# Optimization experiments

Hardware: AMD Instinct MI355X
Metric: run time of the kernel (lower is better)

## Reference

```python
import jax, jax.numpy as jnp
import numpy as np

NEG_INF = -1.0e9  # matches torch masked_fill value

def setup_inputs() -> dict:
    key = jax.random.key(0)
    kq, kk, kv, km = jax.random.split(key, 4)
    B, S, D = 16, 2048, 128
    query = jax.random.normal(kq, (B, S, D), dtype=jnp.float32)
    k = jax.random.normal(kk, (B, S, D), dtype=jnp.float32)
    value = jax.random.normal(kv, (B, S, D), dtype=jnp.float32)
    mask = jax.random.randint(km, (B, S, S), 0, 2).astype(jnp.bool_)
    return {"query": query, "key": k, "value": value, "mask": mask}

def reference(query, key, value, mask):
    # scores: [B, Sq, Sk]
    D = key.shape[-1]
    scale = jnp.sqrt(jnp.asarray(D, dtype=query.dtype))
    scores = jnp.einsum('bqd,bkd->bqk', query, key) / scale
    scores = jnp.where(mask, jnp.asarray(NEG_INF, dtype=scores.dtype), scores)
    attn = jax.nn.softmax(scores, axis=2)
    # dropout p=0.0 -> identity in eval/reference
    out = jnp.einsum('bqk,bkd->bqd', attn, value)
    return out, attn
```

## Files before the change

### kernel.cpp

```cpp
#include <hip/hip_runtime.h>

#define S 2048
#define Dh 128
#define NB 16
#define OUT_ELEMS ((size_t)NB * S * Dh)
#define NEG_BIG -1.0e9f
#define SCALE 0.08838834764831845f

typedef __attribute__((ext_vector_type(8))) short bf16x8;
typedef __attribute__((ext_vector_type(4))) float f32x4;
typedef __attribute__((ext_vector_type(4))) short s16x4;

__device__ __forceinline__ short f2bf(float x) {
    unsigned u = __float_as_uint(x);
    u += 0x7fffu + ((u >> 16) & 1u);
    return (short)(u >> 16);
}

__device__ __forceinline__ s16x4 pack4(float4 v) {
    s16x4 r;
    r.x = f2bf(v.x); r.y = f2bf(v.y); r.z = f2bf(v.z); r.w = f2bf(v.w);
    return r;
}

__global__ void detect_mask(const unsigned char* __restrict__ m, int* __restrict__ flag) {
    __shared__ int any;
    if (threadIdx.x == 0) any = 0;
    __syncthreads();
    int t = threadIdx.x;
    unsigned char v = (unsigned char)(m[t * 4 + 1] | m[t * 4 + 2] | m[t * 4 + 3]);
    if (v) atomicOr(&any, 1);
    __syncthreads();
    if (t == 0) *flag = any;
}

__global__ __launch_bounds__(256) void transpose_v(const float* __restrict__ V,
                                                   short* __restrict__ Vt) {
    const int kb = blockIdx.x, b = blockIdx.y;
    const float* Vb = V + ((size_t)b * S + kb * 64) * Dh;
    short* VtB = Vt + (size_t)b * Dh * S;
    __shared__ float Ls[64][132];
    const int t = threadIdx.x;
#pragma unroll
    for (int i = 0; i < 8; i++) {
        int idx = t + i * 256;
        int r = idx >> 5, c = (idx & 31) << 2;
        *(float4*)&Ls[r][c] = *(const float4*)(Vb + r * Dh + c);
    }
    __syncthreads();
#pragma unroll
    for (int i = 0; i < 8; i++) {
        int idx = t + i * 256;
        int n = idx >> 4, kc = (idx & 15) << 2;
        s16x4 o;
        o.x = f2bf(Ls[kc + 0][n]);
        o.y = f2bf(Ls[kc + 1][n]);
        o.z = f2bf(Ls[kc + 2][n]);
        o.w = f2bf(Ls[kc + 3][n]);
        *(s16x4*)(VtB + (size_t)n * S + kb * 64 + kc) = o;
    }
}

__global__ __launch_bounds__(256) void cvt_bf16(const float* __restrict__ in,
                                                short* __restrict__ out) {
    const size_t n4 = (size_t)NB * S * Dh / 4;
    for (size_t i = (size_t)blockIdx.x * 256 + threadIdx.x; i < n4; i += (size_t)gridDim.x * 256) {
        float4 v = ((const float4*)in)[i];
        ((s16x4*)out)[i] = pack4(v);
    }
}

__global__ __launch_bounds__(256, 2) void flash_pv(const short* __restrict__ Qbf,
                                                   const short* __restrict__ Kbf,
                                                   const short* __restrict__ Vt,
                                                   const void* __restrict__ maskp,
                                                   const int* __restrict__ flagp,
                                                   float2* __restrict__ stats,
                                                   float* __restrict__ Out) {
    const int bid = blockIdx.x;
    const int xcd = bid & 7, kk = bid >> 3;
    const int b = xcd * 2 + (kk >> 5), qt = kk & 31;

    const short* QbfB = Qbf + ((size_t)b * S + qt * 64) * Dh;
    const short* KbfB = Kbf + (size_t)b * S * Dh;
    const short* VtB  = Vt  + (size_t)b * Dh * S;
    float* OutB = Out + ((size_t)b * S + qt * 64) * Dh;
    const int flag = *flagp;

    __shared__ short Qs[2][64][72];
    __shared__ short Ks[2][128][72];
    __shared__ short Ps[2][64][72];
    __shared__ __align__(16) unsigned char Msk[64][128];

    const int t = threadIdx.x, w = t >> 6, lane = t & 63, fr = lane & 15, quad = lane >> 4;
    const int mo = w * 16;

#pragma unroll
    for (int i = 0; i < 4; i++) {
        int idx = t + i * 256;
        int r = idx >> 4, c8 = (idx & 15) * 8;
        *(bf16x8*)&Qs[c8 >> 6][r][c8 & 63] = *(const bf16x8*)(QbfB + (size_t)r * Dh + c8);
    }

    float m[4], l[4];
#pragma unroll
    for (int r = 0; r < 4; r++) { m[r] = -3.4e38f; l[r] = 0.f; }
    f32x4 acc_o[8] = {};

    bf16x8 kv[8];
    int4 mreg[2];
#pragma unroll
    for (int i = 0; i < 8; i++) {
        int idx = t + i * 256;
        int r = idx >> 4, c8 = (idx & 15) * 8;
        kv[i] = *(const bf16x8*)(KbfB + (size_t)r * Dh + c8);
    }
    if (flag) {
        const unsigned char* Mb = (const unsigned char*)maskp + ((size_t)b * S + qt * 64) * S;
#pragma unroll
        for (int i = 0; i < 2; i++) {
            int idx = t + i * 256;
            int r = idx >> 3, c16 = (idx & 7) * 16;
            mreg[i] = *(const int4*)(Mb + (size_t)r * S + c16);
        }
    }

    for (int kt = 0; kt < 16; kt++) {
        __syncthreads();
#pragma unroll
        for (int i = 0; i < 8; i++) {
            int idx = t + i * 256;
            int r = idx >> 4, c8 = (idx & 15) * 8;
            *(bf16x8*)&Ks[c8 >> 6][r][c8 & 63] = kv[i];
        }
        if (flag) {
#pragma unroll
            for (int i = 0; i < 2; i++) {
                int idx = t + i * 256;
                int r = idx >> 3, c16 = (idx & 7) * 16;
                *(int4*)&Msk[r][c16] = mreg[i];
            }
        } else {
            const int* Mb = (const int*)maskp + ((size_t)b * S + qt * 64) * S + (size_t)kt * 128;
#pragma unroll
            for (int i = 0; i < 8; i++) {
                int idx = t + i * 256;
                int r = idx >> 5, c4 = (idx & 31) * 4;
                int4 mv = *(const int4*)(Mb + (size_t)r * S + c4);
                uchar4 o;
                o.x = (unsigned char)(mv.x != 0);
                o.y = (unsigned char)(mv.y != 0);
                o.z = (unsigned char)(mv.z != 0);
                o.w = (unsigned char)(mv.w != 0);
                *(uchar4*)&Msk[r][c4] = o;
            }
        }
        __syncthreads();

        if (kt < 15) {
#pragma unroll
            for (int i = 0; i < 8; i++) {
                int idx = t + i * 256;
                int r = idx >> 4, c8 = (idx & 15) * 8;
                kv[i] = *(const bf16x8*)(KbfB + (size_t)((kt + 1) * 128 + r) * Dh + c8);
            }
            if (flag) {
                const unsigned char* Mb = (const unsigned char*)maskp + ((size_t)b * S + qt * 64) * S + (size_t)(kt + 1) * 128;
#pragma unroll
                for (int i = 0; i < 2; i++) {
                    int idx = t + i * 256;
                    int r = idx >> 3, c16 = (idx & 7) * 16;
                    mreg[i] = *(const int4*)(Mb + (size_t)r * S + c16);
                }
            }
        }

        f32x4 acc_s[8] = {};
#pragma unroll
        for (int ks = 0; ks < 4; ks++) {
            const int h = ks >> 1, o = (ks & 1) * 32 + quad * 8;
            bf16x8 af = *(const bf16x8*)&Qs[h][mo + fr][o];
            bf16x8 bfv[8];
#pragma unroll
            for (int ni = 0; ni < 8; ni++) bfv[ni] = *(const bf16x8*)&Ks[h][ni * 16 + fr][o];
#pragma unroll
            for (int ni = 0; ni < 8; ni++)
                acc_s[ni] = __builtin_amdgcn_mfma_f32_16x16x32_bf16(af, bfv[ni], acc_s[ni], 0, 0, 0);
        }

#pragma unroll
        for (int r = 0; r < 4; r++) {
            const int row = mo + quad * 4 + r;
            float s[8];
#pragma unroll
            for (int ni = 0; ni < 8; ni++) {
                float v = acc_s[ni][r] * SCALE;
                if (Msk[row][ni * 16 + fr]) v = NEG_BIG;
                s[ni] = v;
            }
            float mx = s[0];
#pragma unroll
            for (int ni = 1; ni < 8; ni++) mx = fmaxf(mx, s[ni]);
#pragma unroll
            for (int o = 8; o > 0; o >>= 1) mx = fmaxf(mx, __shfl_xor(mx, o, 64));
            const float mn = fmaxf(m[r], mx);
            const float f = __expf(m[r] - mn);
            float p[8], lt = 0.f;
#pragma unroll
            for (int ni = 0; ni < 8; ni++) { p[ni] = __expf(s[ni] - mn); lt += p[ni]; }
#pragma unroll
            for (int o = 8; o > 0; o >>= 1) lt += __shfl_xor(lt, o, 64);
            l[r] = l[r] * f + lt;
            m[r] = mn;
#pragma unroll
            for (int ni = 0; ni < 8; ni++) acc_o[ni][r] *= f;
#pragma unroll
            for (int ni = 0; ni < 8; ni++) {
                const int col = ni * 16 + fr;
                Ps[col >> 6][row][col & 63] = f2bf(p[ni]);
            }
        }
        __syncthreads();

#pragma unroll
        for (int ks = 0; ks < 4; ks++) {
            const int h = ks >> 1, o = (ks & 1) * 32 + quad * 8;
            bf16x8 paf = *(const bf16x8*)&Ps[h][mo + fr][o];
            bf16x8 pb[8];
#pragma unroll
            for (int ni = 0; ni < 8; ni++)
                pb[ni] = *(const bf16x8*)(VtB + (size_t)(ni * 16 + fr) * S + kt * 128 + ks * 32 + quad * 8);
#pragma unroll
            for (int ni = 0; ni < 8; ni++)
                acc_o[ni] = __builtin_amdgcn_mfma_f32_16x16x32_bf16(paf, pb[ni], acc_o[ni], 0, 0, 0);
        }
    }

    float invl[4];
#pragma unroll
    for (int r = 0; r < 4; r++) invl[r] = 1.0f / l[r];
#pragma unroll
    for (int ni = 0; ni < 8; ni++)
#pragma unroll
        for (int r = 0; r < 4; r++) {
            const int row = mo + quad * 4 + r;
            OutB[(size_t)row * Dh + ni * 16 + fr] = acc_o[ni][r] * invl[r];
        }
    if (fr == 0) {
#pragma unroll
        for (int r = 0; r < 4; r++)
            stats[(size_t)b * S + qt * 64 + mo + quad * 4 + r] = make_float2(m[r], invl[r]);
    }
}

__global__ __launch_bounds__(256, 2) void attn_write(const short* __restrict__ Qbf,
                                                     const short* __restrict__ Kbf,
                                                     const void* __restrict__ maskp,
                                                     const int* __restrict__ flagp,
                                                     const float2* __restrict__ stats,
                                                     float* __restrict__ Attn) {
    const int bid = blockIdx.x;
    const int xcd = bid & 7, kk = bid >> 3;
    const int b = xcd * 2 + (kk >> 8), rem = kk & 255, qt = rem >> 4, kt = rem & 15;

    const short* Qb = Qbf + ((size_t)b * S + qt * 128) * Dh;
    const short* Kb = Kbf + ((size_t)b * S + kt * 128) * Dh;
    __shared__ short As[128][72];
    __shared__ short Bs[128][72];
    __shared__ __align__(16) unsigned char Ms[128][144];
    const int t = threadIdx.x;
    const int w = t >> 6, lane = t & 63, fr = lane & 15, quad = lane >> 4;
    const int mw = (w >> 1) * 64, nw = (w & 1) * 64;
    f32x4 acc[4][4] = {};

    const int flag = *flagp;
    if (flag) {
        const unsigned char* Mb = (const unsigned char*)maskp + ((size_t)b * S + qt * 128) * S + (size_t)kt * 128;
#pragma unroll
        for (int i = 0; i < 4; i++) {
            int idx = t + i * 256;
            int r = idx >> 3, c = (idx & 7) * 16;
            *(int4*)&Ms[r][c] = *(const int4*)(Mb + (size_t)r * S + c);
        }
    } else {
        const int* Mb = (const int*)maskp + ((size_t)b * S + qt * 128) * S + (size_t)kt * 128;
#pragma unroll
        for (int i = 0; i < 16; i++) {
            int idx = t + i * 256;
            int r = idx >> 5, c = (idx & 31) * 4;
            int4 mv = *(const int4*)(Mb + (size_t)r * S + c);
            uchar4 o;
            o.x = (unsigned char)(mv.x != 0);
            o.y = (unsigned char)(mv.y != 0);
            o.z = (unsigned char)(mv.z != 0);
            o.w = (unsigned char)(mv.w != 0);
            *(uchar4*)&Ms[r][c] = o;
        }
    }

    float2 st[4][4];
#pragma unroll
    for (int mi = 0; mi < 4; mi++)
#pragma unroll
        for (int r = 0; r < 4; r++)
            st[mi][r] = stats[(size_t)b * S + qt * 128 + mw + mi * 16 + quad * 4 + r];

    for (int k0 = 0; k0 < Dh; k0 += 64) {
        __syncthreads();
#pragma unroll
        for (int i = 0; i < 4; i++) {
            int idx = t + i * 256;
            int r = idx >> 3, c8 = (idx & 7) * 8;
            *(bf16x8*)&As[r][c8] = *(const bf16x8*)(Qb + (size_t)r * Dh + k0 + c8);
            *(bf16x8*)&Bs[r][c8] = *(const bf16x8*)(Kb + (size_t)r * Dh + k0 + c8);
        }
        __syncthreads();
#pragma unroll
        for (int kc = 0; kc < 2; kc++) {
            const int ko = kc * 32 + quad * 8;
            bf16x8 af[4], bf[4];
#pragma unroll
            for (int mi = 0; mi < 4; mi++) af[mi] = *(const bf16x8*)&As[mw + mi * 16 + fr][ko];
#pragma unroll
            for (int ni = 0; ni < 4; ni++) bf[ni] = *(const bf16x8*)&Bs[nw + ni * 16 + fr][ko];
#pragma unroll
            for (int mi = 0; mi < 4; mi++)
#pragma unroll
                for (int ni = 0; ni < 4; ni++)
                    acc[mi][ni] = __builtin_amdgcn_mfma_f32_16x16x32_bf16(af[mi], bf[ni], acc[mi][ni], 0, 0, 0);
        }
    }

    float* AttnB = Attn + (size_t)b * S * S;
#pragma unroll
    for (int mi = 0; mi < 4; mi++)
#pragma unroll
        for (int ni = 0; ni < 4; ni++)
#pragma unroll
            for (int r = 0; r < 4; r++) {
                const int lrow = mw + mi * 16 + quad * 4 + r;
                const int lcol = nw + ni * 16 + fr;
                float v = acc[mi][ni][r] * SCALE;
                if (Ms[lrow][lcol]) v = NEG_BIG;
                const float p = __expf(v - st[mi][r].x) * st[mi][r].y;
                AttnB[(size_t)(qt * 128 + lrow) * S + kt * 128 + lcol] = p;
            }
}

__global__ __launch_bounds__(256) void reduce_stats(const float2* __restrict__ part,
                                                    float2* __restrict__ stats) {
    const int rid = blockIdx.x * 256 + threadIdx.x;
    const int b = rid >> 11, row = rid & (S - 1);
    float2 p[16];
    float M = -3.4e38f;
#pragma unroll
    for (int kt = 0; kt < 16; kt++) {
        p[kt] = part[((size_t)(b * 16 + kt)) * S + row];
        M = fmaxf(M, p[kt].x);
    }
    float L = 0.f;
#pragma unroll
    for (int kt = 0; kt < 16; kt++) L += p[kt].y * __expf(p[kt].x - M);
    stats[rid] = make_float2(M, 1.0f / L);
}

__global__ __launch_bounds__(256, 2) void qk_kernel(const float* __restrict__ Q,
                                                    const float* __restrict__ Km,
                                                    float* __restrict__ Sc,
                                                    const void* __restrict__ maskp,
                                                    const int* __restrict__ flagp,
                                                    float2* __restrict__ part,
                                                    const int fuse) {
    const int kt = blockIdx.x, qt = blockIdx.y, b = blockIdx.z;
    const float* Qb = Q + ((size_t)b * S + qt * 128) * Dh;
    const float* Kb = Km + ((size_t)b * S + kt * 128) * Dh;
    __shared__ short As[128][72];
    __shared__ short Bs[128][72];
    __shared__ __align__(16) unsigned char Ms[128][144];
    const int t = threadIdx.x;
    const int w = t >> 6, lane = t & 63, fr = lane & 15, quad = lane >> 4;
    const int mw = (w >> 1) * 64, nw = (w & 1) * 64;
    f32x4 acc[4][4] = {};

    if (fuse) {
        const int flag = *flagp;
        if (flag) {
            const unsigned char* Mb = (const unsigned char*)maskp + ((size_t)b * S + qt * 128) * S + (size_t)kt * 128;
#pragma unroll
            for (int i = 0; i < 4; i++) {
                int idx = t + i * 256;
                int r = idx >> 3, c = (idx & 7) * 16;
                *(int4*)&Ms[r][c] = *(const int4*)(Mb + (size_t)r * S + c);
            }
        } else {
            const int* Mb = (const int*)maskp + ((size_t)b * S + qt * 128) * S + (size_t)kt * 128;
#pragma unroll
            for (int i = 0; i < 16; i++) {
                int idx = t + i * 256;
                int r = idx >> 5, c = (idx & 31) * 4;
                int4 mv = *(const int4*)(Mb + (size_t)r * S + c);
                uchar4 o;
                o.x = (unsigned char)(mv.x != 0);
                o.y = (unsigned char)(mv.y != 0);
                o.z = (unsigned char)(mv.z != 0);
                o.w = (unsigned char)(mv.w != 0);
                *(uchar4*)&Ms[r][c] = o;
            }
        }
    }

    for (int k0 = 0; k0 < Dh; k0 += 64) {
        __syncthreads();
#pragma unroll
        for (int i = 0; i < 8; i++) {
            int idx = t + i * 256;
            int r = idx >> 4, c = (idx & 15) << 2;
            float4 qv = *(const float4*)(Qb + r * Dh + k0 + c);
            float4 kv = *(const float4*)(Kb + r * Dh + k0 + c);
            *(s16x4*)&As[r][c] = pack4(qv);
            *(s16x4*)&Bs[r][c] = pack4(kv);
        }
        __syncthreads();
#pragma unroll
        for (int kc = 0; kc < 2; kc++) {
            const int ko = kc * 32 + quad * 8;
            bf16x8 af[4], bf[4];
#pragma unroll
            for (int mi = 0; mi < 4; mi++) af[mi] = *(const bf16x8*)&As[mw + mi * 16 + fr][ko];
#pragma unroll
            for (int ni = 0; ni < 4; ni++) bf[ni] = *(const bf16x8*)&Bs[nw + ni * 16 + fr][ko];
#pragma unroll
            for (int mi = 0; mi < 4; mi++)
#pragma unroll
                for (int ni = 0; ni < 4; ni++)
                    acc[mi][ni] = __builtin_amdgcn_mfma_f32_16x16x32_bf16(af[mi], bf[ni], acc[mi][ni], 0, 0, 0);
        }
    }

    __syncthreads();
    float2* pm = (float2*)&As[0][0];
    float* ScB = Sc + (size_t)b * S * S;
#pragma unroll
    for (int mi = 0; mi < 4; mi++)
#pragma unroll
        for (int r = 0; r < 4; r++) {
            const int lrow = mw + mi * 16 + quad * 4 + r;
            const size_t grow = (size_t)(qt * 128 + lrow);
            float s[4];
#pragma unroll
            for (int ni = 0; ni < 4; ni++) {
                const int lcol = nw + ni * 16 + fr;
                float v = acc[mi][ni][r] * SCALE;
                if (fuse && Ms[lrow][lcol]) v = NEG_BIG;
                s[ni] = v;
                ScB[grow * S + kt * 128 + lcol] = v;
            }
            if (fuse) {
                float mx = fmaxf(fmaxf(s[0], s[1]), fmaxf(s[2], s[3]));
#pragma unroll
                for (int o = 8; o > 0; o >>= 1) mx = fmaxf(mx, __shfl_xor(mx, o, 64));
                float lsum = __expf(s[0] - mx) + __expf(s[1] - mx) +
                             __expf(s[2] - mx) + __expf(s[3] - mx);
#pragma unroll
                for (int o = 8; o > 0; o >>= 1) lsum += __shfl_xor(lsum, o, 64);
                if (fr == 0) pm[lrow * 2 + (w & 1)] = make_float2(mx, lsum);
            }
        }

    if (fuse) {
        __syncthreads();
        if (t < 128) {
            float2 a = pm[t * 2 + 0], c = pm[t * 2 + 1];
            float M = fmaxf(a.x, c.x);
            float L = a.y * __expf(a.x - M) + c.y * __expf(c.x - M);
            part[((size_t)(b * 16 + kt)) * S + qt * 128 + t] = make_float2(M, L);
        }
    }
}

__global__ __launch_bounds__(256) void softmax_kernel(float* __restrict__ Sc,
                                                      const void* __restrict__ maskp,
                                                      const int* __restrict__ flagp) {
    const int b = blockIdx.y;
    const int w = threadIdx.x >> 6, lane = threadIdx.x & 63;
    const int row = blockIdx.x * 4 + w;
    float* R = Sc + ((size_t)b * S + row) * S;
    float4* R4 = (float4*)R;
    const int flag = flagp ? *flagp : 0;

    float sv[32];
    if (flag) {
        const uchar4* M4 = (const uchar4*)((const unsigned char*)maskp + ((size_t)b * S + row) * S);
#pragma unroll
        for (int j = 0; j < 8; j++) {
            float4 v = R4[lane + 64 * j];
            uchar4 mv = M4[lane + 64 * j];
            sv[4 * j + 0] = mv.x ? NEG_BIG : v.x;
            sv[4 * j + 1] = mv.y ? NEG_BIG : v.y;
            sv[4 * j + 2] = mv.z ? NEG_BIG : v.z;
            sv[4 * j + 3] = mv.w ? NEG_BIG : v.w;
        }
    } else {
        const int4* M4 = (const int4*)((const int*)maskp + ((size_t)b * S + row) * S);
#pragma unroll
        for (int j = 0; j < 8; j++) {
            float4 v = R4[lane + 64 * j];
            int4 mv = M4[lane + 64 * j];
            sv[4 * j + 0] = mv.x ? NEG_BIG : v.x;
            sv[4 * j + 1] = mv.y ? NEG_BIG : v.y;
            sv[4 * j + 2] = mv.z ? NEG_BIG : v.z;
            sv[4 * j + 3] = mv.w ? NEG_BIG : v.w;
        }
    }

    float mx = sv[0];
#pragma unroll
    for (int i = 1; i < 32; i++) mx = fmaxf(mx, sv[i]);
    for (int o = 32; o > 0; o >>= 1) mx = fmaxf(mx, __shfl_xor(mx, o, 64));

    float sum = 0.f;
#pragma unroll
    for (int i = 0; i < 32; i++) {
        sv[i] = __expf(sv[i] - mx);
        sum += sv[i];
    }
    for (int o = 32; o > 0; o >>= 1) sum += __shfl_xor(sum, o, 64);
    const float inv = 1.0f / sum;

#pragma unroll
    for (int j = 0; j < 8; j++) {
        float4 p;
        p.x = sv[4 * j + 0] * inv;
        p.y = sv[4 * j + 1] * inv;
        p.z = sv[4 * j + 2] * inv;
        p.w = sv[4 * j + 3] * inv;
        R4[lane + 64 * j] = p;
    }
}

__global__ __launch_bounds__(256, 2) void pv_kernel(float* __restrict__ Sc,
                                                    const float* __restrict__ V,
                                                    const short* __restrict__ Vt,
                                                    const int useVt,
                                                    float* __restrict__ Out,
                                                    const float2* __restrict__ stats,
                                                    const int fuse) {
    const int mt = blockIdx.x, b = blockIdx.y;
    float* ScB = Sc + (size_t)b * S * S + (size_t)mt * 64 * S;
    const float* Vb = V + (size_t)b * S * Dh;
    const short* VtB = Vt + (size_t)b * Dh * S;
    float* OutB = Out + ((size_t)b * S + mt * 64) * Dh;
    __shared__ short As[64][72];
    __shared__ float2 sstat[64];
    const int t = threadIdx.x, w = t >> 6, lane = t & 63, fr = lane & 15, quad = lane >> 4;
    const int mw = (w >> 1) * 32, nw = (w & 1) * 64;
    f32x4 acc[2][4] = {};

    if (fuse && t < 64) sstat[t] = stats[(size_t)b * S + mt * 64 + t];

    for (int k0 = 0; k0 < S; k0 += 64) {
        __syncthreads();
#pragma unroll
        for (int i = 0; i < 4; i++) {
            int idx = t + i * 256;
            int r = idx >> 4, c = (idx & 15) << 2;
            float4 v = *(const float4*)(ScB + (size_t)r * S + k0 + c);
            if (fuse) {
                float2 stv = sstat[r];
                v.x = __expf(v.x - stv.x) * stv.y;
                v.y = __expf(v.y - stv.x) * stv.y;
                v.z = __expf(v.z - stv.x) * stv.y;
                v.w = __expf(v.w - stv.x) * stv.y;
                *(float4*)(ScB + (size_t)r * S + k0 + c) = v;
            }
            *(s16x4*)&As[r][c] = pack4(v);
        }
        __syncthreads();
#pragma unroll
        for (int kc = 0; kc < 2; kc++) {
            const int ko = kc * 32 + quad * 8;
            bf16x8 af[2], bf[4];
#pragma unroll
            for (int mi = 0; mi < 2; mi++) af[mi] = *(const bf16x8*)&As[mw + mi * 16 + fr][ko];
            if (useVt) {
#pragma unroll
                for (int ni = 0; ni < 4; ni++)
                    bf[ni] = *(const bf16x8*)(VtB + (size_t)(nw + ni * 16 + fr) * S + k0 + ko);
            } else {
#pragma unroll
                for (int ni = 0; ni < 4; ni++) {
                    int n = nw + ni * 16 + fr;
#pragma unroll
                    for (int j = 0; j < 8; j++) bf[ni][j] = f2bf(Vb[(size_t)(k0 + ko + j) * Dh + n]);
                }
            }
#pragma unroll
            for (int mi = 0; mi < 2; mi++)
#pragma unroll
                for (int ni = 0; ni < 4; ni++)
                    acc[mi][ni] = __builtin_amdgcn_mfma_f32_16x16x32_bf16(af[mi], bf[ni], acc[mi][ni], 0, 0, 0);
        }
    }

#pragma unroll
    for (int mi = 0; mi < 2; mi++)
#pragma unroll
        for (int ni = 0; ni < 4; ni++)
#pragma unroll
            for (int r = 0; r < 4; r++) {
                int row = mw + mi * 16 + quad * 4 + r;
                int col = nw + ni * 16 + fr;
                OutB[(size_t)row * Dh + col] = acc[mi][ni][r];
            }
}

extern "C" void kernel_launch(void* const* d_in, const int* in_sizes, int n_in,
                              void* d_out, int out_size, void* d_ws, size_t ws_size,
                              hipStream_t stream) {
    const float* Q = (const float*)d_in[0];
    const float* Km = (const float*)d_in[1];
    const float* V = (const float*)d_in[2];
    const void* M = d_in[3];
    float* out = (float*)d_out;
    float* attn = out + OUT_ELEMS;

    const size_t VT_BYTES   = (size_t)NB * Dh * S * sizeof(short);
    const size_t QBF_BYTES  = (size_t)NB * S * Dh * sizeof(short);
    const size_t KBF_BYTES  = QBF_BYTES;
    const size_t STATS_BYTES = (size_t)NB * S * sizeof(float2);
    const size_t REQ_NEW = VT_BYTES + QBF_BYTES + KBF_BYTES + STATS_BYTES + 64;

    if (ws_size >= REQ_NEW) {
        short* Vt   = (short*)d_ws;
        short* Qbf  = (short*)((char*)d_ws + VT_BYTES);
        short* Kbf  = (short*)((char*)d_ws + VT_BYTES + QBF_BYTES);
        float2* stats = (float2*)((char*)d_ws + VT_BYTES + QBF_BYTES + KBF_BYTES);
        int* flag = (int*)((char*)d_ws + VT_BYTES + QBF_BYTES + KBF_BYTES + STATS_BYTES);

        detect_mask<<<1, 256, 0, stream>>>((const unsigned char*)M, flag);
        transpose_v<<<dim3(32, NB), 256, 0, stream>>>(V, Vt);
        cvt_bf16<<<2048, 256, 0, stream>>>(Q, Qbf);
        cvt_bf16<<<2048, 256, 0, stream>>>(Km, Kbf);
        flash_pv<<<512, 256, 0, stream>>>(Qbf, Kbf, Vt, M, flag, stats, out);
        attn_write<<<4096, 256, 0, stream>>>(Qbf, Kbf, M, flag, stats, attn);
        return;
    }

    float2* part = (float2*)d_out;
    int useVt = 0, fuse = 0;
    short* Vt = nullptr;
    float2* stats = nullptr;
    int* flag = nullptr;

    if (ws_size >= VT_BYTES + STATS_BYTES + 64) {
        useVt = 1; fuse = 1;
        Vt = (short*)d_ws;
        stats = (float2*)((char*)d_ws + VT_BYTES);
        flag = (int*)((char*)d_ws + VT_BYTES + STATS_BYTES);
    } else if (ws_size >= VT_BYTES + 64) {
        useVt = 1;
        Vt = (short*)d_ws;
        flag = (int*)((char*)d_ws + VT_BYTES);
    } else if (ws_size >= 64) {
        flag = (int*)d_ws;
    }

    if (flag) detect_mask<<<1, 256, 0, stream>>>((const unsigned char*)M, flag);
    if (useVt) transpose_v<<<dim3(32, NB), 256, 0, stream>>>(V, Vt);

    qk_kernel<<<dim3(16, 16, NB), 256, 0, stream>>>(Q, Km, attn, M, flag, part, fuse);

    if (fuse) {
        reduce_stats<<<dim3((NB * S) / 256), 256, 0, stream>>>(part, stats);
        pv_kernel<<<dim3(32, NB), 256, 0, stream>>>(attn, V, Vt, useVt, out, stats, 1);
    } else {
        softmax_kernel<<<dim3(512, NB), 256, 0, stream>>>(attn, M, flag);
        pv_kernel<<<dim3(32, NB), 256, 0, stream>>>(attn, V, Vt, useVt, out, nullptr, 0);
    }
}
```

Before: 656.3 us.

## Merge prep kernels and load Q/K fragments directly from global memory

Folds the mask detection, V transpose and Q/K bf16 conversion kernels into a single prep launch to cut launch overhead. In flash_pv and attn_write, Q and K MFMA fragments are now read straight from global memory (relying on cache) instead of being staged through shared memory. Each wave also loads only its own mask rows, which lets several block-wide barriers go away. The cost is more global and L2 traffic for K, which is re-read by every wave, and the loss of the software prefetch of the next K tile.

```diff
diff --git a/kernel.cpp b/kernel.cpp
--- a/kernel.cpp
+++ b/kernel.cpp
@@ -34,13 +34,12 @@
     if (t == 0) *flag = any;
 }
 
-__global__ __launch_bounds__(256) void transpose_v(const float* __restrict__ V,
-                                                   short* __restrict__ Vt) {
-    const int kb = blockIdx.x, b = blockIdx.y;
+__device__ __forceinline__ void transpose_v_body(const float* __restrict__ V,
+                                                 short* __restrict__ Vt,
+                                                 int kb, int b, int t,
+                                                 float (*Ls)[132]) {
     const float* Vb = V + ((size_t)b * S + kb * 64) * Dh;
     short* VtB = Vt + (size_t)b * Dh * S;
-    __shared__ float Ls[64][132];
-    const int t = threadIdx.x;
 #pragma unroll
     for (int i = 0; i < 8; i++) {
         int idx = t + i * 256;
@@ -61,12 +60,51 @@
     }
 }
 
+__global__ __launch_bounds__(256) void transpose_v(const float* __restrict__ V,
+                                                   short* __restrict__ Vt) {
+    __shared__ float Ls[64][132];
+    transpose_v_body(V, Vt, blockIdx.x, blockIdx.y, threadIdx.x, Ls);
+}
+
+__device__ __forceinline__ void cvt_body(const float* __restrict__ in,
+                                         short* __restrict__ out,
+                                         int vbid, int nblk, int t) {
+    const size_t n4 = (size_t)NB * S * Dh / 4;
+    for (size_t i = (size_t)vbid * 256 + t; i < n4; i += (size_t)nblk * 256) {
+        float4 v = ((const float4*)in)[i];
+        ((s16x4*)out)[i] = pack4(v);
+    }
+}
+
 __global__ __launch_bounds__(256) void cvt_bf16(const float* __restrict__ in,
                                                 short* __restrict__ out) {
-    const size_t n4 = (size_t)NB * S * Dh / 4;
-    for (size_t i = (size_t)blockIdx.x * 256 + threadIdx.x; i < n4; i += (size_t)gridDim.x * 256) {
-        float4 v = ((const float4*)in)[i];
-        ((s16x4*)out)[i] = pack4(v);
+    cvt_body(in, out, blockIdx.x, gridDim.x, threadIdx.x);
+}
+
+__global__ __launch_bounds__(256) void prep(const float* __restrict__ Q,
+                                            const float* __restrict__ Km,
+                                            const float* __restrict__ V,
+                                            const unsigned char* __restrict__ M,
+                                            short* __restrict__ Qbf,
+                                            short* __restrict__ Kbf,
+                                            short* __restrict__ Vt,
+                                            int* __restrict__ flag) {
+    __shared__ float Ls[64][132];
+    __shared__ int any;
+    const int bid = blockIdx.x, t = threadIdx.x;
+    if (bid < 512) {
+        transpose_v_body(V, Vt, bid & 31, bid >> 5, t, Ls);
+    } else if (bid < 1024) {
+        cvt_body(Q, Qbf, bid - 512, 512, t);
+    } else if (bid < 1536) {
+        cvt_body(Km, Kbf, bid - 1024, 512, t);
+    } else {
+        if (t == 0) any = 0;
+        __syncthreads();
+        unsigned char v = (unsigned char)(M[t * 4 + 1] | M[t * 4 + 2] | M[t * 4 + 3]);
+        if (v) atomicOr(&any, 1);
+        __syncthreads();
+        if (t == 0) *flag = any;
     }
 }
 
@@ -87,105 +125,59 @@
     float* OutB = Out + ((size_t)b * S + qt * 64) * Dh;
     const int flag = *flagp;
 
-    __shared__ short Qs[2][64][72];
-    __shared__ short Ks[2][128][72];
     __shared__ short Ps[2][64][72];
     __shared__ __align__(16) unsigned char Msk[64][128];
 
     const int t = threadIdx.x, w = t >> 6, lane = t & 63, fr = lane & 15, quad = lane >> 4;
     const int mo = w * 16;
 
-#pragma unroll
-    for (int i = 0; i < 4; i++) {
-        int idx = t + i * 256;
-        int r = idx >> 4, c8 = (idx & 15) * 8;
-        *(bf16x8*)&Qs[c8 >> 6][r][c8 & 63] = *(const bf16x8*)(QbfB + (size_t)r * Dh + c8);
-    }
+    bf16x8 af[4];
+#pragma unroll
+    for (int ks = 0; ks < 4; ks++)
+        af[ks] = *(const bf16x8*)(QbfB + (size_t)(mo + fr) * Dh +
+                                  (ks >> 1) * 64 + (ks & 1) * 32 + quad * 8);
 
     float m[4], l[4];
 #pragma unroll
     for (int r = 0; r < 4; r++) { m[r] = -3.4e38f; l[r] = 0.f; }
     f32x4 acc_o[8] = {};
 
-    bf16x8 kv[8];
-    int4 mreg[2];
-#pragma unroll
-    for (int i = 0; i < 8; i++) {
-        int idx = t + i * 256;
-        int r = idx >> 4, c8 = (idx & 15) * 8;
-        kv[i] = *(const bf16x8*)(KbfB + (size_t)r * Dh + c8);
-    }
-    if (flag) {
-        const unsigned char* Mb = (const unsigned char*)maskp + ((size_t)b * S + qt * 64) * S;
-#pragma unroll
-        for (int i = 0; i < 2; i++) {
-            int idx = t + i * 256;
-            int r = idx >> 3, c16 = (idx & 7) * 16;
-            mreg[i] = *(const int4*)(Mb + (size_t)r * S + c16);
-        }
-    }
+    const int mrow = mo + (lane >> 2);
+    const int mcol = (lane & 3) * 32;
+    const size_t mask_row_base = ((size_t)b * S + qt * 64 + mrow) * S;
 
     for (int kt = 0; kt < 16; kt++) {
-        __syncthreads();
-#pragma unroll
-        for (int i = 0; i < 8; i++) {
-            int idx = t + i * 256;
-            int r = idx >> 4, c8 = (idx & 15) * 8;
-            *(bf16x8*)&Ks[c8 >> 6][r][c8 & 63] = kv[i];
-        }
         if (flag) {
-#pragma unroll
-            for (int i = 0; i < 2; i++) {
-                int idx = t + i * 256;
-                int r = idx >> 3, c16 = (idx & 7) * 16;
-                *(int4*)&Msk[r][c16] = mreg[i];
-            }
+            const unsigned char* Mb = (const unsigned char*)maskp + mask_row_base + (size_t)kt * 128 + mcol;
+            int4 a0 = *(const int4*)(Mb);
+            int4 a1 = *(const int4*)(Mb + 16);
+            *(int4*)&Msk[mrow][mcol]      = a0;
+            *(int4*)&Msk[mrow][mcol + 16] = a1;
         } else {
-            const int* Mb = (const int*)maskp + ((size_t)b * S + qt * 64) * S + (size_t)kt * 128;
-#pragma unroll
-            for (int i = 0; i < 8; i++) {
-                int idx = t + i * 256;
-                int r = idx >> 5, c4 = (idx & 31) * 4;
-                int4 mv = *(const int4*)(Mb + (size_t)r * S + c4);
+            const int* Mb = (const int*)maskp + mask_row_base + (size_t)kt * 128 + mcol;
+#pragma unroll
+            for (int j = 0; j < 8; j++) {
+                int4 mv = *(const int4*)(Mb + j * 4);
                 uchar4 o;
                 o.x = (unsigned char)(mv.x != 0);
                 o.y = (unsigned char)(mv.y != 0);
                 o.z = (unsigned char)(mv.z != 0);
                 o.w = (unsigned char)(mv.w != 0);
-                *(uchar4*)&Msk[r][c4] = o;
-            }
-        }
-        __syncthreads();
-
-        if (kt < 15) {
-#pragma unroll
-            for (int i = 0; i < 8; i++) {
-                int idx = t + i * 256;
-                int r = idx >> 4, c8 = (idx & 15) * 8;
-                kv[i] = *(const bf16x8*)(KbfB + (size_t)((kt + 1) * 128 + r) * Dh + c8);
-            }
-            if (flag) {
-                const unsigned char* Mb = (const unsigned char*)maskp + ((size_t)b * S + qt * 64) * S + (size_t)(kt + 1) * 128;
-#pragma unroll
-                for (int i = 0; i < 2; i++) {
-                    int idx = t + i * 256;
-                    int r = idx >> 3, c16 = (idx & 7) * 16;
-                    mreg[i] = *(const int4*)(Mb + (size_t)r * S + c16);
-                }
+                *(uchar4*)&Msk[mrow][mcol + j * 4] = o;
             }
         }
 
         f32x4 acc_s[8] = {};
 #pragma unroll
         for (int ks = 0; ks < 4; ks++) {
-            const int h = ks >> 1, o = (ks & 1) * 32 + quad * 8;
-            bf16x8 af = *(const bf16x8*)&Qs[h][mo + fr][o];
+            const int colk = (ks >> 1) * 64 + (ks & 1) * 32 + quad * 8;
             bf16x8 bfv[8];
 #pragma unroll
-            for (int ni = 0; ni < 8; ni++) bfv[ni] = *(const bf16x8*)&Ks[h][ni * 16 + fr][o];
-#pragma unroll
             for (int ni = 0; ni < 8; ni++)
-                acc_s[ni] = __builtin_amdgcn_mfma_f32_16x16x32_bf16(af, bfv[ni], acc_s[ni], 0, 0, 0);
+                bfv[ni] = *(const bf16x8*)(KbfB + (size_t)(kt * 128 + ni * 16 + fr) * Dh + colk);
+#pragma unroll
+            for (int ni = 0; ni < 8; ni++)
+                acc_s[ni] = __builtin_amdgcn_mfma_f32_16x16x32_bf16(af[ks], bfv[ni], acc_s[ni], 0, 0, 0);
         }
 
 #pragma unroll
@@ -220,12 +212,10 @@
                 Ps[col >> 6][row][col & 63] = f2bf(p[ni]);
             }
         }
-        __syncthreads();
 
 #pragma unroll
         for (int ks = 0; ks < 4; ks++) {
-            const int h = ks >> 1, o = (ks & 1) * 32 + quad * 8;
-            bf16x8 paf = *(const bf16x8*)&Ps[h][mo + fr][o];
+            bf16x8 paf = *(const bf16x8*)&Ps[ks >> 1][mo + fr][(ks & 1) * 32 + quad * 8];
             bf16x8 pb[8];
 #pragma unroll
             for (int ni = 0; ni < 8; ni++)
@@ -263,88 +253,90 @@
     const int xcd = bid & 7, kk = bid >> 3;
     const int b = xcd * 2 + (kk >> 8), rem = kk & 255, qt = rem >> 4, kt = rem & 15;
 
-    const short* Qb = Qbf + ((size_t)b * S + qt * 128) * Dh;
-    const short* Kb = Kbf + ((size_t)b * S + kt * 128) * Dh;
-    __shared__ short As[128][72];
-    __shared__ short Bs[128][72];
-    __shared__ __align__(16) unsigned char Ms[128][144];
-    const int t = threadIdx.x;
-    const int w = t >> 6, lane = t & 63, fr = lane & 15, quad = lane >> 4;
-    const int mw = (w >> 1) * 64, nw = (w & 1) * 64;
-    f32x4 acc[4][4] = {};
-
+    const short* QbfB = Qbf + ((size_t)b * S + qt * 128) * Dh;
+    const short* KbfB = Kbf + ((size_t)b * S + kt * 128) * Dh;
     const int flag = *flagp;
-    if (flag) {
-        const unsigned char* Mb = (const unsigned char*)maskp + ((size_t)b * S + qt * 128) * S + (size_t)kt * 128;
-#pragma unroll
-        for (int i = 0; i < 4; i++) {
-            int idx = t + i * 256;
-            int r = idx >> 3, c = (idx & 7) * 16;
-            *(int4*)&Ms[r][c] = *(const int4*)(Mb + (size_t)r * S + c);
-        }
-    } else {
-        const int* Mb = (const int*)maskp + ((size_t)b * S + qt * 128) * S + (size_t)kt * 128;
-#pragma unroll
-        for (int i = 0; i < 16; i++) {
-            int idx = t + i * 256;
-            int r = idx >> 5, c = (idx & 31) * 4;
-            int4 mv = *(const int4*)(Mb + (size_t)r * S + c);
-            uchar4 o;
-            o.x = (unsigned char)(mv.x != 0);
-            o.y = (unsigned char)(mv.y != 0);
-            o.z = (unsigned char)(mv.z != 0);
-            o.w = (unsigned char)(mv.w != 0);
-            *(uchar4*)&Ms[r][c] = o;
-        }
-    }
-
-    float2 st[4][4];
-#pragma unroll
-    for (int mi = 0; mi < 4; mi++)
+
+    __shared__ __align__(16) unsigned char Msk[128][128];
+
+    const int t = threadIdx.x, w = t >> 6, lane = t & 63, fr = lane & 15, quad = lane >> 4;
+    const int mw = w * 32;
+
+    {
+        const int mcol = (lane & 3) * 32;
+        if (flag) {
+#pragma unroll
+            for (int i = 0; i < 2; i++) {
+                const int row = mw + i * 16 + (lane >> 2);
+                const unsigned char* Mb = (const unsigned char*)maskp +
+                    ((size_t)b * S + qt * 128 + row) * S + (size_t)kt * 128 + mcol;
+                int4 a0 = *(const int4*)(Mb);
+                int4 a1 = *(const int4*)(Mb + 16);
+                *(int4*)&Msk[row][mcol]      = a0;
+                *(int4*)&Msk[row][mcol + 16] = a1;
+            }
+        } else {
+#pragma unroll
+            for (int i = 0; i < 2; i++) {
+                const int row = mw + i * 16 + (lane >> 2);
+                const int* Mb = (const int*)maskp +
+                    ((size_t)b * S + qt * 128 + row) * S + (size_t)kt * 128 + mcol;
+#pragma unroll
+                for (int j = 0; j < 8; j++) {
+                    int4 mv = *(const int4*)(Mb + j * 4);
+                    uchar4 o;
+                    o.x = (unsigned char)(mv.x != 0);
+                    o.y = (unsigned char)(mv.y != 0);
+                    o.z = (unsigned char)(mv.z != 0);
+                    o.w = (unsigned char)(mv.w != 0);
+                    *(uchar4*)&Msk[row][mcol + j * 4] = o;
+                }
+            }
+        }
+    }
+
+    bf16x8 qf[2][4];
+#pragma unroll
+    for (int mi = 0; mi < 2; mi++)
+#pragma unroll
+        for (int ks = 0; ks < 4; ks++)
+            qf[mi][ks] = *(const bf16x8*)(QbfB + (size_t)(mw + mi * 16 + fr) * Dh +
+                                          (ks >> 1) * 64 + (ks & 1) * 32 + quad * 8);
+
+    f32x4 acc[2][8] = {};
+#pragma unroll
+    for (int ks = 0; ks < 4; ks++) {
+        const int colk = (ks >> 1) * 64 + (ks & 1) * 32 + quad * 8;
+        bf16x8 kf[8];
+#pragma unroll
+        for (int ni = 0; ni < 8; ni++)
+            kf[ni] = *(const bf16x8*)(KbfB + (size_t)(ni * 16 + fr) * Dh + colk);
+#pragma unroll
+        for (int mi = 0; mi < 2; mi++)
+#pragma unroll
+            for (int ni = 0; ni < 8; ni++)
+                acc[mi][ni] = __builtin_amdgcn_mfma_f32_16x16x32_bf16(qf[mi][ks], kf[ni], acc[mi][ni], 0, 0, 0);
+    }
+
+    float* AttnB = Attn + (size_t)b * S * S;
+#pragma unroll
+    for (int mi = 0; mi < 2; mi++) {
+        float2 st[4];
 #pragma unroll
         for (int r = 0; r < 4; r++)
-            st[mi][r] = stats[(size_t)b * S + qt * 128 + mw + mi * 16 + quad * 4 + r];
-
-    for (int k0 = 0; k0 < Dh; k0 += 64) {
-        __syncthreads();
-#pragma unroll
-        for (int i = 0; i < 4; i++) {
-            int idx = t + i * 256;
-            int r = idx >> 3, c8 = (idx & 7) * 8;
-            *(bf16x8*)&As[r][c8] = *(const bf16x8*)(Qb + (size_t)r * Dh + k0 + c8);
-            *(bf16x8*)&Bs[r][c8] = *(const bf16x8*)(Kb + (size_t)r * Dh + k0 + c8);
-        }
-        __syncthreads();
-#pragma unroll
-        for (int kc = 0; kc < 2; kc++) {
-            const int ko = kc * 32 + quad * 8;
-            bf16x8 af[4], bf[4];
-#pragma unroll
-            for (int mi = 0; mi < 4; mi++) af[mi] = *(const bf16x8*)&As[mw + mi * 16 + fr][ko];
-#pragma unroll
-            for (int ni = 0; ni < 4; ni++) bf[ni] = *(const bf16x8*)&Bs[nw + ni * 16 + fr][ko];
-#pragma unroll
-            for (int mi = 0; mi < 4; mi++)
-#pragma unroll
-                for (int ni = 0; ni < 4; ni++)
-                    acc[mi][ni] = __builtin_amdgcn_mfma_f32_16x16x32_bf16(af[mi], bf[ni], acc[mi][ni], 0, 0, 0);
-        }
-    }
-
-    float* AttnB = Attn + (size_t)b * S * S;
-#pragma unroll
-    for (int mi = 0; mi < 4; mi++)
-#pragma unroll
-        for (int ni = 0; ni < 4; ni++)
+            st[r] = stats[(size_t)b * S + qt * 128 + mw + mi * 16 + quad * 4 + r];
+#pragma unroll
+        for (int ni = 0; ni < 8; ni++)
 #pragma unroll
             for (int r = 0; r < 4; r++) {
                 const int lrow = mw + mi * 16 + quad * 4 + r;
-                const int lcol = nw + ni * 16 + fr;
+                const int lcol = ni * 16 + fr;
                 float v = acc[mi][ni][r] * SCALE;
-                if (Ms[lrow][lcol]) v = NEG_BIG;
-                const float p = __expf(v - st[mi][r].x) * st[mi][r].y;
+                if (Msk[lrow][lcol]) v = NEG_BIG;
+                const float p = __expf(v - st[r].x) * st[r].y;
                 AttnB[(size_t)(qt * 128 + lrow) * S + kt * 128 + lcol] = p;
             }
+    }
 }
 
 __global__ __launch_bounds__(256) void reduce_stats(const float2* __restrict__ part,
@@ -637,10 +629,7 @@
         float2* stats = (float2*)((char*)d_ws + VT_BYTES + QBF_BYTES + KBF_BYTES);
         int* flag = (int*)((char*)d_ws + VT_BYTES + QBF_BYTES + KBF_BYTES + STATS_BYTES);
 
-        detect_mask<<<1, 256, 0, stream>>>((const unsigned char*)M, flag);
-        transpose_v<<<dim3(32, NB), 256, 0, stream>>>(V, Vt);
-        cvt_bf16<<<2048, 256, 0, stream>>>(Q, Qbf);
-        cvt_bf16<<<2048, 256, 0, stream>>>(Km, Kbf);
+        prep<<<1537, 256, 0, stream>>>(Q, Km, V, (const unsigned char*)M, Qbf, Kbf, Vt, flag);
         flash_pv<<<512, 256, 0, stream>>>(Qbf, Kbf, Vt, M, flag, stats, out);
         attn_write<<<4096, 256, 0, stream>>>(Qbf, Kbf, M, flag, stats, attn);
         return;
```

Measured after the change: 800.2 us. 1.22x slower.
